# Kernel tuning notes

Hardware: AMD Instinct MI355X
Metric: run time of the kernel (lower is better)

## Reference

```python
import jax, jax.numpy as jnp
import numpy as np

B, L, D, H, LAYERS = 4, 1024, 512, 8, 6
HD = D // H           # 64
E = H * HD            # 512 (hid_dim)
F = 4 * D             # 2048 (ffn hidden)
EPS = 1e-5


def _layernorm(x, g, b):
    m = jnp.mean(x, axis=-1, keepdims=True)
    v = jnp.mean((x - m) ** 2, axis=-1, keepdims=True)
    return (x - m) * jax.lax.rsqrt(v + EPS) * g + b


def setup_inputs() -> dict:
    key0 = jax.random.key(0)
    ks = jax.random.split(key0, 20)
    query = jax.random.normal(ks[0], (B, L, D), dtype=jnp.float32)
    key_t = jax.random.normal(ks[1], (B, L, D), dtype=jnp.float32)
    # ragged valid lengths so masking paths are exercised
    lengths = jnp.array([1024, 896, 768, 640], dtype=jnp.int32)
    pos = jnp.arange(L)[None, :]
    query_mask = (pos < lengths[:, None]).astype(jnp.float32)
    key_mask = query_mask
    s = 0.02
    p = {
        'Wq': jax.random.normal(ks[2], (LAYERS, E, D)) * s,
        'bq': jax.random.normal(ks[3], (LAYERS, E)) * s,
        'Wk': jax.random.normal(ks[4], (LAYERS, E, D)) * s,
        'bk': jax.random.normal(ks[5], (LAYERS, E)) * s,
        'Wv': jax.random.normal(ks[6], (LAYERS, E, D)) * s,
        'bv': jax.random.normal(ks[7], (LAYERS, E)) * s,
        'Wo': jax.random.normal(ks[8], (LAYERS, D, E)) * s,
        'bo': jax.random.normal(ks[9], (LAYERS, D)) * s,
        'W1': jax.random.normal(ks[10], (LAYERS, F, D)) * s,
        'b1': jax.random.normal(ks[11], (LAYERS, F)) * s,
        'W2': jax.random.normal(ks[12], (LAYERS, D, F)) * s,
        'b2': jax.random.normal(ks[13], (LAYERS, D)) * s,
        'ln1_g': jnp.ones((LAYERS, D), jnp.float32),
        'ln1_b': jnp.zeros((LAYERS, D), jnp.float32),
        'ln2_g': jnp.ones((LAYERS, D), jnp.float32),
        'ln2_b': jnp.zeros((LAYERS, D), jnp.float32),
    }
    p = {k: v.astype(jnp.float32) for k, v in p.items()}
    return {'query': query, 'key': key_t, 'query_mask': query_mask, 'key_mask': key_mask, **p}


def reference(query, key, query_mask, key_mask,
              Wq, bq, Wk, bk, Wv, bv, Wo, bo,
              W1, b1, W2, b2, ln1_g, ln1_b, ln2_g, ln2_b):
    b, lq, d = query.shape
    scale = jnp.float32(HD) ** -0.5
    kmask0 = (key_mask == 0)[:, None, None, :]  # [B,1,1,Tk]
    qm = query_mask[:, :, None]                  # [B,Tq,1]
    x = query
    for i in range(LAYERS):
        # qkv projections (Conv1d kernel_size=1 == per-token linear)
        q = (jnp.einsum('bld,ed->ble', x, Wq[i]) + bq[i]).reshape(b, lq, H, HD).transpose(0, 2, 1, 3)
        k = (jnp.einsum('bld,ed->ble', key, Wk[i]) + bk[i]).reshape(b, -1, H, HD).transpose(0, 2, 1, 3)
        v = (jnp.einsum('bld,ed->ble', key, Wv[i]) + bv[i]).reshape(b, -1, H, HD).transpose(0, 2, 1, 3)
        scores = jnp.einsum('bhqd,bhkd->bhqk', q * scale, k)  # [B,H,Tq,Tk]
        scores = jnp.where(kmask0, -jnp.inf, scores)
        attn = jax.nn.softmax(scores, axis=-1)
        out = jnp.einsum('bhqk,bhkd->bhqd', attn, v)
        out = out.transpose(0, 2, 1, 3).reshape(b, lq, E)
        out = jnp.einsum('ble,de->bld', out, Wo[i]) + bo[i]
        out = out * qm
        x = _layernorm(out + x, ln1_g[i], ln1_b[i])
        # FFN
        h = jax.nn.relu(jnp.einsum('bld,fd->blf', x, W1[i]) + b1[i])
        f = jnp.einsum('blf,df->bld', h, W2[i]) + b2[i]
        f = f * qm
        x = _layernorm(f + x, ln2_g[i], ln2_b[i])
    return x
```

## Files before the change

kernel.cpp:

```cpp
#include <hip/hip_runtime.h>
#include <stdint.h>

typedef unsigned short u16;
typedef __bf16 bf16_t;
typedef bf16_t v8bf __attribute__((ext_vector_type(8)));
typedef u16    v8u  __attribute__((ext_vector_type(8)));
typedef float  v4f  __attribute__((ext_vector_type(4)));

#define NLAYERS 6
#define LN_EPS 1e-5f
#define NROWS 4096
#define ND 512
#define NF 2048
#define QKV_LD 1536

static constexpr size_t WQKV = 0;
static constexpr size_t WOo  = 4718592;
static constexpr size_t W1o  = 6291456;
static constexpr size_t W2o  = 12582912;
static constexpr size_t BQKV = 18874368;
static constexpr size_t BOo  = BQKV + 9216;
static constexpr size_t B1o  = BOo + 3072;
static constexpr size_t B2o  = B1o + 12288;
static constexpr size_t L1G  = B2o + 3072, L1B = L1G + 3072;
static constexpr size_t L2G  = L1B + 3072, L2B = L2G + 3072;
static constexpr size_t QMo  = L2B + 3072;

__device__ __forceinline__ float b2f(u16 u){
  union { unsigned int i; float f; } x; x.i = ((unsigned int)u) << 16; return x.f;
}
__device__ __forceinline__ u16 f2b(float f){
  union { float f; unsigned int i; } x; x.f = f;
  unsigned int u = x.i;
  return (u16)((u + 0x7fffu + ((u >> 16) & 1u)) >> 16);
}

__device__ __forceinline__ void gl_lds16(const u16* g, u16* l){
  __builtin_amdgcn_global_load_lds(
      (const __attribute__((address_space(1))) unsigned int*)(g),
      (__attribute__((address_space(3))) unsigned int*)(l), 16, 0, 0);
}

__device__ __forceinline__ void cvt8(const float* __restrict__ src, u16* __restrict__ dst){
  float4 x0 = *(const float4*)(src);
  float4 x1 = *(const float4*)(src + 4);
  v8u o;
  o[0]=f2b(x0.x); o[1]=f2b(x0.y); o[2]=f2b(x0.z); o[3]=f2b(x0.w);
  o[4]=f2b(x1.x); o[5]=f2b(x1.y); o[6]=f2b(x1.z); o[7]=f2b(x1.w);
  *(v8u*)dst = o;
}

__global__ __launch_bounds__(256) void conv_qk(
    const float* __restrict__ q, const float* __restrict__ k,
    u16* __restrict__ xb, u16* __restrict__ kcan)
{
  const int i = (blockIdx.x * 256 + threadIdx.x) * 8;
  if (i < 2097152) cvt8(q + i, xb + i);
  else             cvt8(k + (i - 2097152), kcan + (i - 2097152));
}

__global__ __launch_bounds__(256) void conv_qkvw(
    const float* __restrict__ wq, const float* __restrict__ wk,
    const float* __restrict__ wv, u16* __restrict__ wcan)
{
  const int i = (blockIdx.x * 256 + threadIdx.x) * 8;
  const float* src; int part, j;
  if (i < 1572864){ part = 0; j = i;           src = wq + j; }
  else if (i < 3145728){ part = 1; j = i - 1572864; src = wk + j; }
  else { part = 2; j = i - 3145728; src = wv + j; }
  const int layer = j >> 18, within = j & 262143;
  cvt8(src, wcan + WQKV + (size_t)layer * 786432 + part * 262144 + within);
}

__global__ __launch_bounds__(256) void conv_w3(
    const float* __restrict__ wo, const float* __restrict__ w1,
    const float* __restrict__ w2, u16* __restrict__ wcan)
{
  const int i = (blockIdx.x * 256 + threadIdx.x) * 8;
  if (i < 1572864)      cvt8(wo + i, wcan + WOo + i);
  else if (i < 7864320) cvt8(w1 + (i - 1572864), wcan + W1o + (i - 1572864));
  else                  cvt8(w2 + (i - 7864320), wcan + W2o + (i - 7864320));
}

__global__ __launch_bounds__(256) void conv_small(
    const float* __restrict__ bqs, const float* __restrict__ bks,
    const float* __restrict__ bvs, const float* __restrict__ bos,
    const float* __restrict__ b1s, const float* __restrict__ b2s,
    const float* __restrict__ g1,  const float* __restrict__ be1,
    const float* __restrict__ g2,  const float* __restrict__ be2,
    const float* __restrict__ qm,  u16* __restrict__ wcan)
{
  const int v = blockIdx.x * 256 + threadIdx.x;
  if (v >= 5504) return;
  const int i = v * 8;
  const float* src; size_t dst;
  if (i < 9216){
    const int part = i / 3072;
    const int j = i - part * 3072;
    src = (part == 0 ? bqs : part == 1 ? bks : bvs) + j;
    dst = BQKV + (size_t)(j >> 9) * 1536 + part * 512 + (j & 511);
  } else if (i < 12288){ const int j = i -  9216; src = bos + j; dst = BOo + j; }
  else if (i < 24576){ const int j = i - 12288; src = b1s + j; dst = B1o + j; }
  else if (i < 27648){ const int j = i - 24576; src = b2s + j; dst = B2o + j; }
  else if (i < 30720){ const int j = i - 27648; src = g1  + j; dst = L1G + j; }
  else if (i < 33792){ const int j = i - 30720; src = be1 + j; dst = L1B + j; }
  else if (i < 36864){ const int j = i - 33792; src = g2  + j; dst = L2G + j; }
  else if (i < 39936){ const int j = i - 36864; src = be2 + j; dst = L2B + j; }
  else               { const int j = i - 39936; src = qm  + j; dst = QMo + j; }
  cvt8(src, wcan + dst);
}

__global__ void compute_len(const float* __restrict__ qm, int* __restrict__ len){
  __shared__ int cnt;
  if (threadIdx.x == 0) cnt = 0;
  __syncthreads();
  int c = 0;
  const int b = blockIdx.x;
  for (int i = threadIdx.x; i < 1024; i += 256)
    if (qm[b * 1024 + i] != 0.f) c++;
  atomicAdd(&cnt, c);
  __syncthreads();
  if (threadIdx.x == 0) len[b] = cnt;
}

template<int MT, int NT, int RELU, int QKV>
__global__ __launch_bounds__(256) void gemm_k(
    const u16* __restrict__ A0, const u16* __restrict__ A1,
    const u16* __restrict__ W, const u16* __restrict__ bias,
    u16* __restrict__ C, u16* __restrict__ VT,
    const int* __restrict__ len_g, int ldc, int K)
{
  constexpr int WM = MT / 2, WN = NT / 2;
  constexpr int NI = WM / 16, NJ = WN / 16;
  constexpr int RA = MT / 64, RB = NT / 64;
  __shared__ __align__(16) u16 As[MT * 32];
  __shared__ __align__(16) u16 Bs[NT * 32];

  const int t    = threadIdx.x;
  const int lane = t & 63, wave = t >> 6;
  const int ln   = lane & 15, quad = lane >> 4;
  const int n0 = blockIdx.x * NT;
  const int m0 = blockIdx.y * MT;
  if ((m0 & 1023) >= len_g[m0 >> 10]) return;

  const u16* A = (QKV && n0 >= 512) ? A1 : A0;
  const int wm = wave & 1, wn = wave >> 1;
  const int sw = (quad + (ln >> 1)) & 3;

  v4f acc[NI][NJ];
  #pragma unroll
  for (int i = 0; i < NI; ++i)
    #pragma unroll
    for (int j = 0; j < NJ; ++j) acc[i][j] = (v4f){0.f,0.f,0.f,0.f};

  const u16* aS[RA]; const u16* bS[RB];
  #pragma unroll
  for (int ra = 0; ra < RA; ++ra){
    const int u = t + ra * 256;
    const int c = ((u & 3) - (u >> 3)) & 3;
    aS[ra] = A + (size_t)(m0 + (u >> 2)) * K + c * 8;
  }
  #pragma unroll
  for (int rb = 0; rb < RB; ++rb){
    const int u = t + rb * 256;
    const int c = ((u & 3) - (u >> 3)) & 3;
    bS[rb] = W + (size_t)(n0 + (u >> 2)) * K + c * 8;
  }

  for (int k0 = 0; k0 < K; k0 += 32){
    #pragma unroll
    for (int ra = 0; ra < RA; ++ra) gl_lds16(aS[ra] + k0, &As[(t + ra*256) * 8]);
    #pragma unroll
    for (int rb = 0; rb < RB; ++rb) gl_lds16(bS[rb] + k0, &Bs[(t + rb*256) * 8]);
    __syncthreads();

    v8bf a[NI], bf[NJ];
    #pragma unroll
    for (int i = 0; i < NI; ++i)
      a[i] = *(const v8bf*)&As[(wm * WM + i * 16 + ln) * 32 + sw * 8];
    #pragma unroll
    for (int j = 0; j < NJ; ++j)
      bf[j] = *(const v8bf*)&Bs[(wn * WN + j * 16 + ln) * 32 + sw * 8];
    #pragma unroll
    for (int i = 0; i < NI; ++i)
      #pragma unroll
      for (int j = 0; j < NJ; ++j)
        acc[i][j] = __builtin_amdgcn_mfma_f32_16x16x32_bf16(a[i], bf[j], acc[i][j], 0, 0, 0);
    __syncthreads();
  }

  #pragma unroll
  for (int j = 0; j < NJ; ++j){
    const int col = n0 + wn * WN + j * 16 + ln;
    const float bs = b2f(bias[col]);
    #pragma unroll
    for (int i = 0; i < NI; ++i){
      #pragma unroll
      for (int r = 0; r < 4; ++r){
        const int row = m0 + wm * WM + i * 16 + quad * 4 + r;
        float v = acc[i][j][r] + bs;
        if (RELU) v = fmaxf(v, 0.f);
        if (QKV && col >= 1024){
          const int e = col - 1024;
          VT[(((size_t)(row >> 10) * 8 + (e >> 6)) * 64 + (e & 63)) * 1024 + (row & 1023)] = f2b(v);
        } else {
          C[(size_t)row * ldc + col] = f2b(v);
        }
      }
    }
  }
}

__global__ __launch_bounds__(256) void attn_kernel(
    const u16* __restrict__ qkv, const u16* __restrict__ VT,
    const int* __restrict__ len_g, u16* __restrict__ O)
{
  __shared__ __align__(16) u16 Ks[64 * 72];
  __shared__ __align__(16) u16 Vs[64 * 72];
  __shared__ __align__(16) u16 Pl[4][16 * 72];

  const int t    = threadIdx.x;
  const int lane = t & 63, wave = t >> 6;
  const int ln   = lane & 15, quad = lane >> 4;
  const int bh = blockIdx.x >> 4;
  const int qc = blockIdx.x & 15;
  const int h = bh & 7, b = bh >> 3;
  const int len = len_g[b];
  if (qc * 64 >= len) return;
  const int q0 = qc * 64 + wave * 16;

  const u16* Qb = qkv + ((size_t)b * 1024 + q0 + ln) * QKV_LD + h * 64;
  const v8bf aq0 = *(const v8bf*)(Qb + quad * 8);
  const v8bf aq1 = *(const v8bf*)(Qb + 32 + quad * 8);

  const u16* Kbase = qkv + (size_t)b * 1024 * QKV_LD + 512 + h * 64;
  const u16* Vbase = VT + (size_t)bh * 64 * 1024;

  const int r0 = t >> 3,         c0 = (t & 7) * 8;
  const int r1 = (t + 256) >> 3, c1 = c0;
  const u16* Kst0 = Kbase + (size_t)r0 * QKV_LD + c0;
  const u16* Kst1 = Kbase + (size_t)r1 * QKV_LD + c1;
  const u16* Vst0 = Vbase + (size_t)r0 * 1024 + c0;
  const u16* Vst1 = Vbase + (size_t)r1 * 1024 + c1;
  u16* KsD0 = &Ks[r0 * 72 + c0]; u16* KsD1 = &Ks[r1 * 72 + c1];
  u16* VsD0 = &Vs[r0 * 72 + c0]; u16* VsD1 = &Vs[r1 * 72 + c1];

  float m_i[4], l_i[4];
  #pragma unroll
  for (int r = 0; r < 4; ++r){ m_i[r] = -1e30f; l_i[r] = 0.f; }
  v4f o_acc[4];
  #pragma unroll
  for (int c = 0; c < 4; ++c) o_acc[c] = (v4f){0.f,0.f,0.f,0.f};

  u16* P = Pl[wave];

  v8u ck0 = *(const v8u*)Kst0;
  v8u ck1 = *(const v8u*)Kst1;
  v8u cv0 = *(const v8u*)Vst0;
  v8u cv1 = *(const v8u*)Vst1;

  for (int j0 = 0; j0 < len; j0 += 64){
    __syncthreads();
    *(v8u*)KsD0 = ck0; *(v8u*)KsD1 = ck1;
    *(v8u*)VsD0 = cv0; *(v8u*)VsD1 = cv1;
    __syncthreads();

    const int jn = j0 + 64;
    if (jn < len){
      ck0 = *(const v8u*)(Kst0 + (size_t)jn * QKV_LD);
      ck1 = *(const v8u*)(Kst1 + (size_t)jn * QKV_LD);
      cv0 = *(const v8u*)(Vst0 + jn);
      cv1 = *(const v8u*)(Vst1 + jn);
    }

    const bool tail = (len - j0) < 64;

    v4f s[4];
    #pragma unroll
    for (int st = 0; st < 4; ++st){
      const u16* kr = &Ks[(st * 16 + ln) * 72];
      v4f ss = {0.f,0.f,0.f,0.f};
      ss = __builtin_amdgcn_mfma_f32_16x16x32_bf16(aq0, *(const v8bf*)(kr + quad * 8),      ss, 0,0,0);
      ss = __builtin_amdgcn_mfma_f32_16x16x32_bf16(aq1, *(const v8bf*)(kr + 32 + quad * 8), ss, 0,0,0);
      s[st] = ss;
    }

    float p[4][4], mt[4];
    #pragma unroll
    for (int r = 0; r < 4; ++r) mt[r] = -1e30f;
    #pragma unroll
    for (int st = 0; st < 4; ++st){
      const bool dead = tail && (j0 + st * 16 + ln) >= len;
      #pragma unroll
      for (int r = 0; r < 4; ++r){
        float sc = dead ? -1e30f : s[st][r] * 0.125f;
        p[st][r] = sc;
        mt[r] = fmaxf(mt[r], sc);
      }
    }
    #pragma unroll
    for (int off = 1; off < 16; off <<= 1)
      #pragma unroll
      for (int r = 0; r < 4; ++r) mt[r] = fmaxf(mt[r], __shfl_xor(mt[r], off));

    float alpha[4], ts[4];
    #pragma unroll
    for (int r = 0; r < 4; ++r){
      const float mn = fmaxf(m_i[r], mt[r]);
      alpha[r] = __expf(m_i[r] - mn);
      m_i[r] = mn;
    }
    #pragma unroll
    for (int st = 0; st < 4; ++st)
      #pragma unroll
      for (int r = 0; r < 4; ++r) p[st][r] = __expf(p[st][r] - m_i[r]);
    #pragma unroll
    for (int r = 0; r < 4; ++r) ts[r] = (p[0][r] + p[1][r]) + (p[2][r] + p[3][r]);
    #pragma unroll
    for (int off = 1; off < 16; off <<= 1)
      #pragma unroll
      for (int r = 0; r < 4; ++r) ts[r] += __shfl_xor(ts[r], off);
    #pragma unroll
    for (int r = 0; r < 4; ++r) l_i[r] = l_i[r] * alpha[r] + ts[r];
    #pragma unroll
    for (int c = 0; c < 4; ++c)
      #pragma unroll
      for (int r = 0; r < 4; ++r) o_acc[c][r] *= alpha[r];

    #pragma unroll
    for (int st = 0; st < 4; ++st)
      #pragma unroll
      for (int r = 0; r < 4; ++r)
        P[(quad * 4 + r) * 72 + st * 16 + ln] = f2b(p[st][r]);
    const v8bf ap0 = *(const v8bf*)&P[ln * 72 + quad * 8];
    const v8bf ap1 = *(const v8bf*)&P[ln * 72 + 32 + quad * 8];

    #pragma unroll
    for (int c = 0; c < 4; ++c){
      const u16* vr = &Vs[(c * 16 + ln) * 72];
      o_acc[c] = __builtin_amdgcn_mfma_f32_16x16x32_bf16(ap0, *(const v8bf*)(vr + quad * 8),      o_acc[c], 0,0,0);
      o_acc[c] = __builtin_amdgcn_mfma_f32_16x16x32_bf16(ap1, *(const v8bf*)(vr + 32 + quad * 8), o_acc[c], 0,0,0);
    }
  }

  u16* Ob = O + ((size_t)b * 1024 + q0) * 512 + h * 64;
  #pragma unroll
  for (int c = 0; c < 4; ++c)
    #pragma unroll
    for (int r = 0; r < 4; ++r)
      Ob[(size_t)(quad * 4 + r) * 512 + c * 16 + ln] = f2b(o_acc[c][r] / l_i[r]);
}

template<int OUT>
__global__ __launch_bounds__(256) void ln_res(
    const u16* __restrict__ Y, const u16* __restrict__ qm,
    const u16* __restrict__ g, const u16* __restrict__ beta,
    u16* __restrict__ X, float* __restrict__ fout)
{
  const int lane = threadIdx.x & 63;
  const int wave = threadIdx.x >> 6;
  const int row  = blockIdx.x * 4 + wave;

  const float qv = b2f(qm[row]);
  const u16* y = Y + (size_t)row * ND;
  u16*       x = X + (size_t)row * ND;

  v8u yv = *(const v8u*)(y + lane * 8);
  v8u xv = *(const v8u*)(x + lane * 8);
  float tt[8]; float s = 0.f, s2 = 0.f;
  #pragma unroll
  for (int i = 0; i < 8; ++i){
    tt[i] = b2f(yv[i]) * qv + b2f(xv[i]);
    s  += tt[i];
    s2 += tt[i] * tt[i];
  }
  #pragma unroll
  for (int off = 1; off < 64; off <<= 1){
    s  += __shfl_xor(s,  off);
    s2 += __shfl_xor(s2, off);
  }
  const float mean = s * (1.f / ND);
  const float var  = fmaxf(s2 * (1.f / ND) - mean * mean, 0.f);
  const float inv  = rsqrtf(var + LN_EPS);

  v8u gv = *(const v8u*)(g    + lane * 8);
  v8u bv = *(const v8u*)(beta + lane * 8);
  float ov[8];
  #pragma unroll
  for (int i = 0; i < 8; ++i)
    ov[i] = (tt[i] - mean) * inv * b2f(gv[i]) + b2f(bv[i]);

  if (OUT){
    float4 o0, o1;
    o0.x=ov[0]; o0.y=ov[1]; o0.z=ov[2]; o0.w=ov[3];
    o1.x=ov[4]; o1.y=ov[5]; o1.z=ov[6]; o1.w=ov[7];
    float* fo = fout + (size_t)row * ND + lane * 8;
    *(float4*)fo = o0;
    *(float4*)(fo + 4) = o1;
  } else {
    v8u o;
    #pragma unroll
    for (int i = 0; i < 8; ++i) o[i] = f2b(ov[i]);
    *(v8u*)(x + lane * 8) = o;
  }
}

extern "C" void kernel_launch(void* const* d_in, const int* in_sizes, int n_in,
                              void* d_out, int out_size, void* d_ws, size_t ws_size,
                              hipStream_t stream)
{
  char* ws = (char*)d_ws;
  const size_t MiB = 1u << 20;
  u16* qkv = (u16*)(ws);
  u16* VT  = (u16*)(ws + 12 * MiB);
  u16* hb  = (u16*)(ws);
  u16* tb1 = (u16*)(ws);
  u16* xb   = (u16*)(ws + 16 * MiB);
  u16* kcan = (u16*)(ws + 20 * MiB);
  u16* ob   = (u16*)(ws + 24 * MiB);
  u16* tb2  = ob;
  u16* wcan = (u16*)(ws + 28 * MiB);
  int* len  = (int*)(ws + 65 * MiB);

  const float* f_qm = (const float*)d_in[2];

  conv_qk<<<2048, 256, 0, stream>>>((const float*)d_in[0], (const float*)d_in[1], xb, kcan);
  conv_qkvw<<<2304, 256, 0, stream>>>((const float*)d_in[4], (const float*)d_in[6],
                                      (const float*)d_in[8], wcan);
  conv_w3<<<6912, 256, 0, stream>>>((const float*)d_in[10], (const float*)d_in[12],
                                    (const float*)d_in[14], wcan);
  conv_small<<<22, 256, 0, stream>>>(
      (const float*)d_in[5],  (const float*)d_in[7],  (const float*)d_in[9],
      (const float*)d_in[11], (const float*)d_in[13], (const float*)d_in[15],
      (const float*)d_in[16], (const float*)d_in[17],
      (const float*)d_in[18], (const float*)d_in[19], f_qm, wcan);
  compute_len<<<4, 256, 0, stream>>>(f_qm, len);

  for (int i = 0; i < NLAYERS; ++i){
    const u16* Wqkv_i = wcan + WQKV + (size_t)i * 786432;
    const u16* bqkv_i = wcan + BQKV + (size_t)i * 1536;
    const u16* Wo_i = wcan + WOo + (size_t)i * 262144;
    const u16* W1_i = wcan + W1o + (size_t)i * 1048576;
    const u16* W2_i = wcan + W2o + (size_t)i * 1048576;

    gemm_k<64,128,0,1><<<dim3(12, 64), 256, 0, stream>>>(
        xb, kcan, Wqkv_i, bqkv_i, qkv, VT, len, QKV_LD, ND);

    attn_kernel<<<512, 256, 0, stream>>>(qkv, VT, len, ob);

    gemm_k<64,64,0,0><<<dim3(8, 64), 256, 0, stream>>>(
        ob, ob, Wo_i, wcan + BOo + (size_t)i * ND, tb1, nullptr, len, ND, ND);
    ln_res<0><<<NROWS / 4, 256, 0, stream>>>(tb1, wcan + QMo,
        wcan + L1G + (size_t)i * ND, wcan + L1B + (size_t)i * ND, xb, nullptr);

    gemm_k<128,128,1,0><<<dim3(16, 32), 256, 0, stream>>>(
        xb, xb, W1_i, wcan + B1o + (size_t)i * NF, hb, nullptr, len, NF, ND);
    gemm_k<64,64,0,0><<<dim3(8, 64), 256, 0, stream>>>(
        hb, hb, W2_i, wcan + B2o + (size_t)i * ND, tb2, nullptr, len, ND, NF);

    if (i < NLAYERS - 1)
      ln_res<0><<<NROWS / 4, 256, 0, stream>>>(tb2, wcan + QMo,
          wcan + L2G + (size_t)i * ND, wcan + L2B + (size_t)i * ND, xb, nullptr);
    else
      ln_res<1><<<NROWS / 4, 256, 0, stream>>>(tb2, wcan + QMo,
          wcan + L2G + (size_t)i * ND, wcan + L2B + (size_t)i * ND, xb, (float*)d_out);
  }
}
```

Before: 817.5 us.

## Hoist K/V projections out of layer loop, fuse Q projection into attention, split-K Wo/W2

K and V depend only on the fixed key input, so all six layers' K/V projections are computed in one batched launch before the loop instead of a QKV GEMM per layer. The Q projection for each head/query tile is computed inside the attention kernel via MFMA, which removes the qkv buffer round-trip. The Wo and W2 GEMMs become split-K kernels writing fp32 partials, and the LayerNorm kernel sums the partials and adds the bias, raising parallelism for these narrow-N GEMMs. The cost is extra fp32 partial traffic and more workspace for the per-layer K/V buffers.

```diff
diff --git a/kernel.cpp b/kernel.cpp
--- a/kernel.cpp
+++ b/kernel.cpp
@@ -12,7 +12,6 @@
 #define NROWS 4096
 #define ND 512
 #define NF 2048
-#define QKV_LD 1536
 
 static constexpr size_t WQKV = 0;
 static constexpr size_t WOo  = 4718592;
@@ -34,13 +33,11 @@
   unsigned int u = x.i;
   return (u16)((u + 0x7fffu + ((u >> 16) & 1u)) >> 16);
 }
-
 __device__ __forceinline__ void gl_lds16(const u16* g, u16* l){
   __builtin_amdgcn_global_load_lds(
       (const __attribute__((address_space(1))) unsigned int*)(g),
       (__attribute__((address_space(3))) unsigned int*)(l), 16, 0, 0);
 }
-
 __device__ __forceinline__ void cvt8(const float* __restrict__ src, u16* __restrict__ dst){
   float4 x0 = *(const float4*)(src);
   float4 x1 = *(const float4*)(src + 4);
@@ -123,11 +120,10 @@
   if (threadIdx.x == 0) len[b] = cnt;
 }
 
-template<int MT, int NT, int RELU, int QKV>
+template<int MT, int NT, int RELU>
 __global__ __launch_bounds__(256) void gemm_k(
-    const u16* __restrict__ A0, const u16* __restrict__ A1,
-    const u16* __restrict__ W, const u16* __restrict__ bias,
-    u16* __restrict__ C, u16* __restrict__ VT,
+    const u16* __restrict__ A, const u16* __restrict__ W,
+    const u16* __restrict__ bias, u16* __restrict__ C,
     const int* __restrict__ len_g, int ldc, int K)
 {
   constexpr int WM = MT / 2, WN = NT / 2;
@@ -143,7 +139,6 @@
   const int m0 = blockIdx.y * MT;
   if ((m0 & 1023) >= len_g[m0 >> 10]) return;
 
-  const u16* A = (QKV && n0 >= 512) ? A1 : A0;
   const int wm = wave & 1, wn = wave >> 1;
   const int sw = (quad + (ln >> 1)) & 3;
 
@@ -200,20 +195,160 @@
         const int row = m0 + wm * WM + i * 16 + quad * 4 + r;
         float v = acc[i][j][r] + bs;
         if (RELU) v = fmaxf(v, 0.f);
-        if (QKV && col >= 1024){
-          const int e = col - 1024;
-          VT[(((size_t)(row >> 10) * 8 + (e >> 6)) * 64 + (e & 63)) * 1024 + (row & 1023)] = f2b(v);
+        C[(size_t)row * ldc + col] = f2b(v);
+      }
+    }
+  }
+}
+
+__global__ __launch_bounds__(256) void gemm_kv(
+    const u16* __restrict__ kcan, const u16* __restrict__ wcan,
+    const int* __restrict__ len_g, u16* __restrict__ Kall, u16* __restrict__ VTall)
+{
+  __shared__ __align__(16) u16 As[64 * 32];
+  __shared__ __align__(16) u16 Bs[128 * 32];
+
+  const int t    = threadIdx.x;
+  const int lane = t & 63, wave = t >> 6;
+  const int ln   = lane & 15, quad = lane >> 4;
+  const int layer = blockIdx.z;
+  const int n0 = blockIdx.x * 128;
+  const int m0 = blockIdx.y * 64;
+  if ((m0 & 1023) >= len_g[m0 >> 10]) return;
+
+  const u16* W    = wcan + WQKV + (size_t)layer * 786432;
+  const u16* bias = wcan + BQKV + (size_t)layer * 1536 + 512;
+  u16* Kl  = Kall  + (size_t)layer * 2097152;
+  u16* VTl = VTall + (size_t)layer * 2097152;
+
+  const int wm = wave & 1, wn = wave >> 1;
+  const int sw = (quad + (ln >> 1)) & 3;
+
+  v4f acc[2][4];
+  #pragma unroll
+  for (int i = 0; i < 2; ++i)
+    #pragma unroll
+    for (int j = 0; j < 4; ++j) acc[i][j] = (v4f){0.f,0.f,0.f,0.f};
+
+  const int cA = ((t & 3) - (t >> 3)) & 3;
+  const u16* aS0 = kcan + (size_t)(m0 + (t >> 2)) * 512 + cA * 8;
+  const u16* bS0 = W + (size_t)(512 + n0 + (t >> 2)) * 512 + cA * 8;
+  const int u1 = t + 256;
+  const int cB = ((u1 & 3) - (u1 >> 3)) & 3;
+  const u16* bS1 = W + (size_t)(512 + n0 + (u1 >> 2)) * 512 + cB * 8;
+
+  for (int k0 = 0; k0 < 512; k0 += 32){
+    gl_lds16(aS0 + k0, &As[t * 8]);
+    gl_lds16(bS0 + k0, &Bs[t * 8]);
+    gl_lds16(bS1 + k0, &Bs[u1 * 8]);
+    __syncthreads();
+
+    v8bf a[2], bf[4];
+    #pragma unroll
+    for (int i = 0; i < 2; ++i)
+      a[i] = *(const v8bf*)&As[(wm * 32 + i * 16 + ln) * 32 + sw * 8];
+    #pragma unroll
+    for (int j = 0; j < 4; ++j)
+      bf[j] = *(const v8bf*)&Bs[(wn * 64 + j * 16 + ln) * 32 + sw * 8];
+    #pragma unroll
+    for (int i = 0; i < 2; ++i)
+      #pragma unroll
+      for (int j = 0; j < 4; ++j)
+        acc[i][j] = __builtin_amdgcn_mfma_f32_16x16x32_bf16(a[i], bf[j], acc[i][j], 0, 0, 0);
+    __syncthreads();
+  }
+
+  #pragma unroll
+  for (int j = 0; j < 4; ++j){
+    const int col = n0 + wn * 64 + j * 16 + ln;
+    const float bs = b2f(bias[col]);
+    #pragma unroll
+    for (int i = 0; i < 2; ++i){
+      #pragma unroll
+      for (int r = 0; r < 4; ++r){
+        const int row = m0 + wm * 32 + i * 16 + quad * 4 + r;
+        const float v = acc[i][j][r] + bs;
+        if (col < 512){
+          Kl[(size_t)row * 512 + col] = f2b(v);
         } else {
-          C[(size_t)row * ldc + col] = f2b(v);
+          const int e = col - 512;
+          VTl[(((size_t)(row >> 10) * 8 + (e >> 6)) * 64 + (e & 63)) * 1024 + (row & 1023)] = f2b(v);
         }
       }
     }
   }
 }
 
+template<int KS>
+__global__ __launch_bounds__(256) void gemm_split(
+    const u16* __restrict__ A, const u16* __restrict__ W,
+    float* __restrict__ part, const int* __restrict__ len_g, int K)
+{
+  __shared__ __align__(16) u16 As[64 * 32];
+  __shared__ __align__(16) u16 Bs[64 * 32];
+
+  const int t    = threadIdx.x;
+  const int lane = t & 63, wave = t >> 6;
+  const int ln   = lane & 15, quad = lane >> 4;
+  const int n0 = blockIdx.x * 64;
+  const int m0 = blockIdx.y * 64;
+  const int z  = blockIdx.z;
+  if ((m0 & 1023) >= len_g[m0 >> 10]) return;
+
+  const int wm = wave & 1, wn = wave >> 1;
+  const int sw = (quad + (ln >> 1)) & 3;
+  const int ks0 = z * KS;
+
+  v4f acc[2][2];
+  #pragma unroll
+  for (int i = 0; i < 2; ++i)
+    #pragma unroll
+    for (int j = 0; j < 2; ++j) acc[i][j] = (v4f){0.f,0.f,0.f,0.f};
+
+  const int c = ((t & 3) - (t >> 3)) & 3;
+  const u16* aS = A + (size_t)(m0 + (t >> 2)) * K + ks0 + c * 8;
+  const u16* bS = W + (size_t)(n0 + (t >> 2)) * K + ks0 + c * 8;
+
+  for (int k0 = 0; k0 < KS; k0 += 32){
+    gl_lds16(aS + k0, &As[t * 8]);
+    gl_lds16(bS + k0, &Bs[t * 8]);
+    __syncthreads();
+
+    v8bf a[2], bf[2];
+    #pragma unroll
+    for (int i = 0; i < 2; ++i)
+      a[i] = *(const v8bf*)&As[(wm * 32 + i * 16 + ln) * 32 + sw * 8];
+    #pragma unroll
+    for (int j = 0; j < 2; ++j)
+      bf[j] = *(const v8bf*)&Bs[(wn * 32 + j * 16 + ln) * 32 + sw * 8];
+    #pragma unroll
+    for (int i = 0; i < 2; ++i)
+      #pragma unroll
+      for (int j = 0; j < 2; ++j)
+        acc[i][j] = __builtin_amdgcn_mfma_f32_16x16x32_bf16(a[i], bf[j], acc[i][j], 0, 0, 0);
+    __syncthreads();
+  }
+
+  float* pz = part + (size_t)z * 2097152;
+  #pragma unroll
+  for (int j = 0; j < 2; ++j){
+    const int col = n0 + wn * 32 + j * 16 + ln;
+    #pragma unroll
+    for (int i = 0; i < 2; ++i){
+      #pragma unroll
+      for (int r = 0; r < 4; ++r){
+        const int row = m0 + wm * 32 + i * 16 + quad * 4 + r;
+        pz[(size_t)row * 512 + col] = acc[i][j][r];
+      }
+    }
+  }
+}
+
 __global__ __launch_bounds__(256) void attn_kernel(
-    const u16* __restrict__ qkv, const u16* __restrict__ VT,
-    const int* __restrict__ len_g, u16* __restrict__ O)
+    const u16* __restrict__ xb, const u16* __restrict__ Wq,
+    const u16* __restrict__ bq, const u16* __restrict__ Kl,
+    const u16* __restrict__ VTl, const int* __restrict__ len_g,
+    u16* __restrict__ O)
 {
   __shared__ __align__(16) u16 Ks[64 * 72];
   __shared__ __align__(16) u16 Vs[64 * 72];
@@ -229,36 +364,62 @@
   if (qc * 64 >= len) return;
   const int q0 = qc * 64 + wave * 16;
 
-  const u16* Qb = qkv + ((size_t)b * 1024 + q0 + ln) * QKV_LD + h * 64;
-  const v8bf aq0 = *(const v8bf*)(Qb + quad * 8);
-  const v8bf aq1 = *(const v8bf*)(Qb + 32 + quad * 8);
-
-  const u16* Kbase = qkv + (size_t)b * 1024 * QKV_LD + 512 + h * 64;
-  const u16* Vbase = VT + (size_t)bh * 64 * 1024;
-
   const int r0 = t >> 3,         c0 = (t & 7) * 8;
   const int r1 = (t + 256) >> 3, c1 = c0;
-  const u16* Kst0 = Kbase + (size_t)r0 * QKV_LD + c0;
-  const u16* Kst1 = Kbase + (size_t)r1 * QKV_LD + c1;
-  const u16* Vst0 = Vbase + (size_t)r0 * 1024 + c0;
-  const u16* Vst1 = Vbase + (size_t)r1 * 1024 + c1;
+  const u16* Kst0 = Kl + (size_t)(b * 1024 + r0) * 512 + h * 64 + c0;
+  const u16* Kst1 = Kl + (size_t)(b * 1024 + r1) * 512 + h * 64 + c1;
+  const u16* Vst0 = VTl + (size_t)bh * 65536 + (size_t)r0 * 1024 + c0;
+  const u16* Vst1 = VTl + (size_t)bh * 65536 + (size_t)r1 * 1024 + c1;
   u16* KsD0 = &Ks[r0 * 72 + c0]; u16* KsD1 = &Ks[r1 * 72 + c1];
   u16* VsD0 = &Vs[r0 * 72 + c0]; u16* VsD1 = &Vs[r1 * 72 + c1];
-
-  float m_i[4], l_i[4];
-  #pragma unroll
-  for (int r = 0; r < 4; ++r){ m_i[r] = -1e30f; l_i[r] = 0.f; }
-  v4f o_acc[4];
-  #pragma unroll
-  for (int c = 0; c < 4; ++c) o_acc[c] = (v4f){0.f,0.f,0.f,0.f};
-
-  u16* P = Pl[wave];
 
   v8u ck0 = *(const v8u*)Kst0;
   v8u ck1 = *(const v8u*)Kst1;
   v8u cv0 = *(const v8u*)Vst0;
   v8u cv1 = *(const v8u*)Vst1;
 
+  const int sw = (quad + (ln >> 1)) & 3;
+  const int cA = ((t & 3) - (t >> 3)) & 3;
+  const u16* xS = xb + (size_t)(b * 1024 + qc * 64 + (t >> 2)) * 512 + cA * 8;
+  const u16* wS = Wq + (size_t)(h * 64 + (t >> 2)) * 512 + cA * 8;
+
+  v4f qa[4];
+  #pragma unroll
+  for (int j = 0; j < 4; ++j) qa[j] = (v4f){0.f,0.f,0.f,0.f};
+
+  for (int k0 = 0; k0 < 512; k0 += 32){
+    gl_lds16(xS + k0, &Ks[t * 8]);
+    gl_lds16(wS + k0, &Vs[t * 8]);
+    __syncthreads();
+    v8bf ax = *(const v8bf*)&Ks[(wave * 16 + ln) * 32 + sw * 8];
+    v8bf bw[4];
+    #pragma unroll
+    for (int j = 0; j < 4; ++j)
+      bw[j] = *(const v8bf*)&Vs[(j * 16 + ln) * 32 + sw * 8];
+    #pragma unroll
+    for (int j = 0; j < 4; ++j)
+      qa[j] = __builtin_amdgcn_mfma_f32_16x16x32_bf16(ax, bw[j], qa[j], 0, 0, 0);
+    __syncthreads();
+  }
+
+  u16* P = Pl[wave];
+  #pragma unroll
+  for (int j = 0; j < 4; ++j){
+    const float bs = b2f(bq[h * 64 + j * 16 + ln]);
+    #pragma unroll
+    for (int r = 0; r < 4; ++r)
+      P[(quad * 4 + r) * 72 + j * 16 + ln] = f2b(qa[j][r] + bs);
+  }
+  const v8bf aq0 = *(const v8bf*)&P[ln * 72 + quad * 8];
+  const v8bf aq1 = *(const v8bf*)&P[ln * 72 + 32 + quad * 8];
+
+  float m_i[4], l_i[4];
+  #pragma unroll
+  for (int r = 0; r < 4; ++r){ m_i[r] = -1e30f; l_i[r] = 0.f; }
+  v4f o_acc[4];
+  #pragma unroll
+  for (int c = 0; c < 4; ++c) o_acc[c] = (v4f){0.f,0.f,0.f,0.f};
+
   for (int j0 = 0; j0 < len; j0 += 64){
     __syncthreads();
     *(v8u*)KsD0 = ck0; *(v8u*)KsD1 = ck1;
@@ -267,8 +428,8 @@
 
     const int jn = j0 + 64;
     if (jn < len){
-      ck0 = *(const v8u*)(Kst0 + (size_t)jn * QKV_LD);
-      ck1 = *(const v8u*)(Kst1 + (size_t)jn * QKV_LD);
+      ck0 = *(const v8u*)(Kst0 + (size_t)jn * 512);
+      ck1 = *(const v8u*)(Kst1 + (size_t)jn * 512);
       cv0 = *(const v8u*)(Vst0 + jn);
       cv1 = *(const v8u*)(Vst1 + jn);
     }
@@ -351,35 +512,48 @@
       Ob[(size_t)(quad * 4 + r) * 512 + c * 16 + ln] = f2b(o_acc[c][r] / l_i[r]);
 }
 
-template<int OUT>
+template<int S, int OUT>
 __global__ __launch_bounds__(256) void ln_res(
-    const u16* __restrict__ Y, const u16* __restrict__ qm,
-    const u16* __restrict__ g, const u16* __restrict__ beta,
-    u16* __restrict__ X, float* __restrict__ fout)
+    const float* __restrict__ part, const u16* __restrict__ bias,
+    const u16* __restrict__ qm, const u16* __restrict__ g,
+    const u16* __restrict__ beta, u16* __restrict__ X, float* __restrict__ fout)
 {
   const int lane = threadIdx.x & 63;
   const int wave = threadIdx.x >> 6;
   const int row  = blockIdx.x * 4 + wave;
 
   const float qv = b2f(qm[row]);
-  const u16* y = Y + (size_t)row * ND;
-  u16*       x = X + (size_t)row * ND;
-
-  v8u yv = *(const v8u*)(y + lane * 8);
+  u16* x = X + (size_t)row * ND;
+
+  const float* pr = part + (size_t)row * 512 + lane * 8;
+  float y[8];
+  {
+    v8u bvv = *(const v8u*)(bias + lane * 8);
+    #pragma unroll
+    for (int i = 0; i < 8; ++i) y[i] = b2f(bvv[i]);
+  }
+  #pragma unroll
+  for (int s = 0; s < S; ++s){
+    float4 a0 = *(const float4*)(pr + (size_t)s * 2097152);
+    float4 a1 = *(const float4*)(pr + (size_t)s * 2097152 + 4);
+    y[0]+=a0.x; y[1]+=a0.y; y[2]+=a0.z; y[3]+=a0.w;
+    y[4]+=a1.x; y[5]+=a1.y; y[6]+=a1.z; y[7]+=a1.w;
+  }
+
   v8u xv = *(const v8u*)(x + lane * 8);
-  float tt[8]; float s = 0.f, s2 = 0.f;
+  float tt[8]; float s1 = 0.f, s2 = 0.f;
   #pragma unroll
   for (int i = 0; i < 8; ++i){
-    tt[i] = b2f(yv[i]) * qv + b2f(xv[i]);
-    s  += tt[i];
+    tt[i] = y[i] * qv + b2f(xv[i]);
+    s1 += tt[i];
     s2 += tt[i] * tt[i];
   }
   #pragma unroll
   for (int off = 1; off < 64; off <<= 1){
-    s  += __shfl_xor(s,  off);
+    s1 += __shfl_xor(s1, off);
     s2 += __shfl_xor(s2, off);
   }
-  const float mean = s * (1.f / ND);
+  const float mean = s1 * (1.f / ND);
   const float var  = fmaxf(s2 * (1.f / ND) - mean * mean, 0.f);
   const float inv  = rsqrtf(var + LN_EPS);
 
@@ -411,16 +585,15 @@
 {
   char* ws = (char*)d_ws;
   const size_t MiB = 1u << 20;
-  u16* qkv = (u16*)(ws);
-  u16* VT  = (u16*)(ws + 12 * MiB);
-  u16* hb  = (u16*)(ws);
-  u16* tb1 = (u16*)(ws);
-  u16* xb   = (u16*)(ws + 16 * MiB);
-  u16* kcan = (u16*)(ws + 20 * MiB);
-  u16* ob   = (u16*)(ws + 24 * MiB);
-  u16* tb2  = ob;
-  u16* wcan = (u16*)(ws + 28 * MiB);
-  int* len  = (int*)(ws + 65 * MiB);
+  u16*   hb    = (u16*)(ws);
+  float* part  = (float*)(ws + 16 * MiB);
+  u16*   xb    = (u16*)(ws + 48 * MiB);
+  u16*   kcan  = (u16*)(ws + 52 * MiB);
+  u16*   ob    = (u16*)(ws + 56 * MiB);
+  u16*   wcan  = (u16*)(ws + 60 * MiB);
+  u16*   Kall  = (u16*)(ws + 98 * MiB);
+  u16*   VTall = (u16*)(ws + 122 * MiB);
+  int*   len   = (int*)(ws + 146 * MiB);
 
   const float* f_qm = (const float*)d_in[2];
 
@@ -436,33 +609,32 @@
       (const float*)d_in[18], (const float*)d_in[19], f_qm, wcan);
   compute_len<<<4, 256, 0, stream>>>(f_qm, len);
 
+  gemm_kv<<<dim3(8, 64, 6), 256, 0, stream>>>(kcan, wcan, len, Kall, VTall);
+
   for (int i = 0; i < NLAYERS; ++i){
-    const u16* Wqkv_i = wcan + WQKV + (size_t)i * 786432;
-    const u16* bqkv_i = wcan + BQKV + (size_t)i * 1536;
+    const u16* Wq_i = wcan + WQKV + (size_t)i * 786432;
+    const u16* bq_i = wcan + BQKV + (size_t)i * 1536;
     const u16* Wo_i = wcan + WOo + (size_t)i * 262144;
     const u16* W1_i = wcan + W1o + (size_t)i * 1048576;
     const u16* W2_i = wcan + W2o + (size_t)i * 1048576;
-
-    gemm_k<64,128,0,1><<<dim3(12, 64), 256, 0, stream>>>(
-        xb, kcan, Wqkv_i, bqkv_i, qkv, VT, len, QKV_LD, ND);
-
-    attn_kernel<<<512, 256, 0, stream>>>(qkv, VT, len, ob);
-
-    gemm_k<64,64,0,0><<<dim3(8, 64), 256, 0, stream>>>(
-        ob, ob, Wo_i, wcan + BOo + (size_t)i * ND, tb1, nullptr, len, ND, ND);
-    ln_res<0><<<NROWS / 4, 256, 0, stream>>>(tb1, wcan + QMo,
-        wcan + L1G + (size_t)i * ND, wcan + L1B + (size_t)i * ND, xb, nullptr);
-
-    gemm_k<128,128,1,0><<<dim3(16, 32), 256, 0, stream>>>(
-        xb, xb, W1_i, wcan + B1o + (size_t)i * NF, hb, nullptr, len, NF, ND);
-    gemm_k<64,64,0,0><<<dim3(8, 64), 256, 0, stream>>>(
-        hb, hb, W2_i, wcan + B2o + (size_t)i * ND, tb2, nullptr, len, ND, NF);
-
+    const u16* Kl   = Kall  + (size_t)i * 2097152;
+    const u16* VTl  = VTall + (size_t)i * 2097152;
+
+    attn_kernel<<<512, 256, 0, stream>>>(xb, Wq_i, bq_i, Kl, VTl, len, ob);
+
+    gemm_split<256><<<dim3(8, 64, 2), 256, 0, stream>>>(ob, Wo_i, part, len, ND);
+    ln_res<2,0><<<NROWS / 4, 256, 0, stream>>>(part, wcan + BOo + (size_t)i * ND,
+        wcan + QMo, wcan + L1G + (size_t)i * ND, wcan + L1B + (size_t)i * ND, xb, nullptr);
+
+    gemm_k<128,128,1><<<dim3(16, 32), 256, 0, stream>>>(
+        xb, W1_i, wcan + B1o + (size_t)i * NF, hb, len, NF, ND);
+
+    gemm_split<512><<<dim3(8, 64, 4), 256, 0, stream>>>(hb, W2_i, part, len, NF);
     if (i < NLAYERS - 1)
-      ln_res<0><<<NROWS / 4, 256, 0, stream>>>(tb2, wcan + QMo,
-          wcan + L2G + (size_t)i * ND, wcan + L2B + (size_t)i * ND, xb, nullptr);
+      ln_res<4,0><<<NROWS / 4, 256, 0, stream>>>(part, wcan + B2o + (size_t)i * ND,
+          wcan + QMo, wcan + L2G + (size_t)i * ND, wcan + L2B + (size_t)i * ND, xb, nullptr);
     else
-      ln_res<1><<<NROWS / 4, 256, 0, stream>>>(tb2, wcan + QMo,
-          wcan + L2G + (size_t)i * ND, wcan + L2B + (size_t)i * ND, xb, (float*)d_out);
-  }
-}
+      ln_res<4,1><<<NROWS / 4, 256, 0, stream>>>(part, wcan + B2o + (size_t)i * ND,
+          wcan + QMo, wcan + L2G + (size_t)i * ND, wcan + L2B + (size_t)i * ND, xb, (float*)d_out);
+  }
+}
```

Result: slower. 834.5 us (+2.1%).
